# Kernel tuning notes

Hardware: AMD Instinct MI355X
Metric: run time of the kernel (lower is better)

The kernel has to match this reference:

```python
import jax, jax.numpy as jnp
import numpy as np

BETA_MIN = 1e-06


def setup_inputs() -> dict:
    key = jax.random.key(0)
    ks = jax.random.split(key, 4)
    B, H, W, C = 32, 56, 56, 256
    x = jax.random.normal(ks[0], (B, H, W, C), dtype=jnp.float32)
    # NonNeg-constrained weights, init value gamma_init = 1/16
    gamma_k = jax.random.uniform(ks[1], (1, 1, 8, C), dtype=jnp.float32) * (1.0 / 16.0)
    gamma_s = jax.random.uniform(ks[2], (3, 3, C, 1), dtype=jnp.float32) * (1.0 / 16.0)
    beta = jax.random.uniform(ks[3], (C,), dtype=jnp.float32) * 1e-06
    beta_outside = jnp.zeros((C,), dtype=jnp.float32)
    gamma_outside = jnp.ones((C,), dtype=jnp.float32)
    return {
        'x': x,
        'gamma_k': gamma_k,
        'gamma_s': gamma_s,
        'beta': beta,
        'beta_outside': beta_outside,
        'gamma_outside': gamma_outside,
        'surround_dist': 1,
    }


def reference(x, gamma_k, gamma_s, beta, beta_outside, gamma_outside, surround_dist):
    B, H, W, C = x.shape
    G = C // 8  # norm_groups = C / 8, 8 channels per group

    x2 = x * x

    # Grouped 1x1 conv: gamma_k[0,0] is [8, C]; group g uses columns g*8:(g+1)*8
    # reshape to [in=8, group, out=8] and contract per group.
    w = gamma_k[0, 0].reshape(8, G, 8)  # [i, g, o]
    Pk = jnp.einsum('bhwgi,igo->bhwgo', x2.reshape(B, H, W, G, 8), w)
    Pk = Pk.reshape(B, H, W, C)

    # Masked (center-zero) dilated 3x3 depthwise conv on squared inputs.
    mask = jnp.array([[1.0, 1.0, 1.0], [1.0, 0.0, 1.0], [1.0, 1.0, 1.0]], dtype=x.dtype)
    k = gamma_s[..., 0] * mask[:, :, None]  # [3, 3, C]
    kern = k[:, :, None, :]  # HWIO with I = C/groups = 1, O = C
    Ps = jax.lax.conv_general_dilated(
        x2, kern,
        window_strides=(1, 1),
        padding='SAME',
        rhs_dilation=(surround_dist, surround_dist),
        dimension_numbers=('NHWC', 'HWIO', 'NHWC'),
        feature_group_count=C,
    )

    # Divisive normalization: x / sqrt(Pk + Ps + beta + beta_min), then affine.
    norm_pool = jnp.reciprocal(jnp.sqrt(Pk + Ps + (beta + BETA_MIN)))
    return x * norm_pool * gamma_outside + beta_outside
```

## Files before the change

### kernel.cpp

```cpp
#include <hip/hip_runtime.h>

typedef float floatx4 __attribute__((ext_vector_type(4)));

#define BB 32
#define HH 56
#define WW 56
#define CC 256
#define PSTRIP 4
#define WSTRIPS 14
#define HTILE 4
#define HTILES 14
#define BLOCKS_PER_IMG (HTILES * WSTRIPS)

__global__ __launch_bounds__(256) void dn_kernel(
    const float* __restrict__ x,
    const float* __restrict__ gk_g,
    const float* __restrict__ gs_g,
    const float* __restrict__ beta,
    const float* __restrict__ beta_o,
    const float* __restrict__ gamma_o,
    const int* __restrict__ sdist,
    float* __restrict__ out)
{
    __shared__ float lw[20 * CC];

    const int tid = threadIdx.x;

    for (int idx = tid; idx < 19 * 64; idx += 256) {
        const int r  = idx >> 6;
        const int cq = (idx & 63) << 2;
        floatx4 v;
        if (r < 8) {
            v = *reinterpret_cast<const floatx4*>(gk_g + r * CC + cq);
        } else if (r < 16) {
            const int t   = r - 8;
            const int pos = t + (t >= 4 ? 1 : 0);
            v = *reinterpret_cast<const floatx4*>(gs_g + pos * CC + cq);
        } else if (r == 16) {
            v = *reinterpret_cast<const floatx4*>(beta + cq);
            v += 1e-6f;
        } else if (r == 17) {
            v = *reinterpret_cast<const floatx4*>(gamma_o + cq);
        } else {
            v = *reinterpret_cast<const floatx4*>(beta_o + cq);
        }
        *reinterpret_cast<floatx4*>(&lw[r * CC + cq]) = v;
    }

    const int d    = sdist[0];
    const int xcd  = blockIdx.x & 7;
    const int q    = blockIdx.x >> 3;
    const int b    = xcd + ((q / BLOCKS_PER_IMG) << 3);
    const int t0   = q % BLOCKS_PER_IMG;
    const int h    = (t0 / WSTRIPS) * HTILE + (tid >> 6);
    const int w0   = (t0 % WSTRIPS) * PSTRIP;
    const int lane = tid & 63;
    const int c0   = lane << 2;
    const int cg   = c0 & ~7;

    const float* xb   = x + (size_t)b * HH * WW * CC;
    const float* row0 = xb + (size_t)h * WW * CC;
    float*       orow = out + ((size_t)(b * HH + h) * WW) * CC;
    const float* wk   = lw + c0;

    const int  hm  = h - d, hp = h + d;
    const bool rmv = (unsigned)hm < HH;
    const bool rpv = (unsigned)hp < HH;
    const float* rowm = xb + (long)hm * (WW * CC);
    const float* rowp = xb + (long)hp * (WW * CC);
    const int cdm = -d * CC;
    const int cdp =  d * CC;

    __syncthreads();

    const floatx4 zero = {0.f, 0.f, 0.f, 0.f};

#pragma unroll
    for (int j = 0; j < PSTRIP; ++j) {
        const int w = w0 + j;
        const bool wmv = (w - d) >= 0;
        const bool wpv = (w + d) < WW;
        const float* cp = row0 + w * CC;
        const float* mp = rowm + w * CC;
        const float* pp = rowp + w * CC;

        floatx4 cxa = *reinterpret_cast<const floatx4*>(cp + cg);
        floatx4 cxb = *reinterpret_cast<const floatx4*>(cp + cg + 4);

        floatx4 tp[4];
        tp[0] = (rmv && wmv) ? *reinterpret_cast<const floatx4*>(mp + cdm + c0) : zero;
        tp[1] =  rmv         ? *reinterpret_cast<const floatx4*>(mp       + c0) : zero;
        tp[2] = (rmv && wpv) ? *reinterpret_cast<const floatx4*>(mp + cdp + c0) : zero;
        tp[3] =         wmv  ? *reinterpret_cast<const floatx4*>(cp + cdm + c0) : zero;

        const floatx4 cxo = (lane & 1) ? cxb : cxa;
        const floatx4 sqa = cxa * cxa, sqb = cxb * cxb;
        floatx4 acc = *reinterpret_cast<const floatx4*>(wk + 16 * CC);
#pragma unroll
        for (int i = 0; i < 4; ++i)
            acc += sqa[i] * *reinterpret_cast<const floatx4*>(wk + i * CC);
#pragma unroll
        for (int i = 0; i < 4; ++i)
            acc += sqb[i] * *reinterpret_cast<const floatx4*>(wk + (4 + i) * CC);

#pragma unroll
        for (int tt = 0; tt < 4; ++tt)
            acc += (tp[tt] * tp[tt]) *
                   *reinterpret_cast<const floatx4*>(wk + (8 + tt) * CC);

        tp[0] =         wpv  ? *reinterpret_cast<const floatx4*>(cp + cdp + c0) : zero;
        tp[1] = (rpv && wmv) ? *reinterpret_cast<const floatx4*>(pp + cdm + c0) : zero;
        tp[2] =  rpv         ? *reinterpret_cast<const floatx4*>(pp       + c0) : zero;
        tp[3] = (rpv && wpv) ? *reinterpret_cast<const floatx4*>(pp + cdp + c0) : zero;

#pragma unroll
        for (int tt = 0; tt < 4; ++tt)
            acc += (tp[tt] * tp[tt]) *
                   *reinterpret_cast<const floatx4*>(wk + (12 + tt) * CC);

        const floatx4 gov = *reinterpret_cast<const floatx4*>(wk + 17 * CC);
        const floatx4 bov = *reinterpret_cast<const floatx4*>(wk + 18 * CC);
        floatx4 res;
#pragma unroll
        for (int o = 0; o < 4; ++o)
            res[o] = cxo[o] * __builtin_amdgcn_rsqf(acc[o]) * gov[o] + bov[o];

        __builtin_nontemporal_store(res,
            reinterpret_cast<floatx4*>(orow + w * CC + c0));
    }
}

extern "C" void kernel_launch(void* const* d_in, const int* in_sizes, int n_in,
                              void* d_out, int out_size, void* d_ws, size_t ws_size,
                              hipStream_t stream) {
    const float* x       = (const float*)d_in[0];
    const float* gamma_k = (const float*)d_in[1];
    const float* gamma_s = (const float*)d_in[2];
    const float* beta    = (const float*)d_in[3];
    const float* beta_o  = (const float*)d_in[4];
    const float* gamma_o = (const float*)d_in[5];
    const int*   sdist   = (const int*)d_in[6];
    float* out = (float*)d_out;

    const int blocks = BB * BLOCKS_PER_IMG;
    dn_kernel<<<blocks, 256, 0, stream>>>(x, gamma_k, gamma_s, beta,
                                          beta_o, gamma_o, sdist, out);
}
```

Measured before the change: 227.6 us.

## Split channels across two waves per row and make neighbor loads branchless

Each wavefront now handles half of the channels at two channels per lane, and the tile height drops from four rows to two, which doubles the number of blocks. The eight neighbor loads for the depthwise stencil are now unconditional: their indices are clamped and the loaded values are multiplied by 0/1 validity masks instead of being loaded under a branch. The aim is more parallelism, lower register pressure and no divergent predicated loads. In exchange, loads narrow to 8 bytes, the weight table is loaded from global memory into LDS for twice as many blocks, and out-of-range loads are redundant but remain in bounds.

Result: slower. 263.2 us (+15.6%).

```diff
diff --git a/kernel.cpp b/kernel.cpp
--- a/kernel.cpp
+++ b/kernel.cpp
@@ -1,6 +1,7 @@
 #include <hip/hip_runtime.h>
 
 typedef float floatx4 __attribute__((ext_vector_type(4)));
+typedef float floatx2 __attribute__((ext_vector_type(2)));
 
 #define BB 32
 #define HH 56
@@ -8,8 +9,8 @@
 #define CC 256
 #define PSTRIP 4
 #define WSTRIPS 14
-#define HTILE 4
-#define HTILES 14
+#define HTILE 2
+#define HTILES 28
 #define BLOCKS_PER_IMG (HTILES * WSTRIPS)
 
 __global__ __launch_bounds__(256) void dn_kernel(
@@ -52,81 +53,89 @@
     const int q    = blockIdx.x >> 3;
     const int b    = xcd + ((q / BLOCKS_PER_IMG) << 3);
     const int t0   = q % BLOCKS_PER_IMG;
-    const int h    = (t0 / WSTRIPS) * HTILE + (tid >> 6);
+    const int wid  = tid >> 6;
+    const int h    = (t0 / WSTRIPS) * HTILE + (wid >> 1);
     const int w0   = (t0 % WSTRIPS) * PSTRIP;
+    const int half = wid & 1;
     const int lane = tid & 63;
-    const int c0   = lane << 2;
+    const int c0   = (half << 7) + (lane << 1);
     const int cg   = c0 & ~7;
 
-    const float* xb   = x + (size_t)b * HH * WW * CC;
-    const float* row0 = xb + (size_t)h * WW * CC;
+    const float* xb = x + (size_t)b * HH * WW * CC;
+
+    const int hm  = h - d, hp = h + d;
+    const float vrm = (hm >= 0) ? 1.f : 0.f;
+    const float vrp = (hp < HH) ? 1.f : 0.f;
+    const int hmc = (hm >= 0) ? hm : 0;
+    const int hpc = (hp < HH) ? hp : (HH - 1);
+    const float* rowm = xb + (size_t)hmc * (WW * CC);
+    const float* row0 = xb + (size_t)h   * (WW * CC);
+    const float* rowp = xb + (size_t)hpc * (WW * CC);
     float*       orow = out + ((size_t)(b * HH + h) * WW) * CC;
     const float* wk   = lw + c0;
 
-    const int  hm  = h - d, hp = h + d;
-    const bool rmv = (unsigned)hm < HH;
-    const bool rpv = (unsigned)hp < HH;
-    const float* rowm = xb + (long)hm * (WW * CC);
-    const float* rowp = xb + (long)hp * (WW * CC);
-    const int cdm = -d * CC;
-    const int cdp =  d * CC;
-
     __syncthreads();
-
-    const floatx4 zero = {0.f, 0.f, 0.f, 0.f};
 
 #pragma unroll
     for (int j = 0; j < PSTRIP; ++j) {
-        const int w = w0 + j;
-        const bool wmv = (w - d) >= 0;
-        const bool wpv = (w + d) < WW;
-        const float* cp = row0 + w * CC;
-        const float* mp = rowm + w * CC;
-        const float* pp = rowp + w * CC;
+        const int w  = w0 + j;
+        const int wm = w - d, wp = w + d;
+        const float vwm = (wm >= 0) ? 1.f : 0.f;
+        const float vwp = (wp < WW) ? 1.f : 0.f;
+        const int wmc = (wm >= 0) ? wm : 0;
+        const int wpc = (wp < WW) ? wp : (WW - 1);
+        const int colm = wmc * CC + c0;
+        const int col0 = w   * CC + c0;
+        const int colp = wpc * CC + c0;
 
-        floatx4 cxa = *reinterpret_cast<const floatx4*>(cp + cg);
-        floatx4 cxb = *reinterpret_cast<const floatx4*>(cp + cg + 4);
+        floatx2 t0v = *reinterpret_cast<const floatx2*>(rowm + colm);
+        floatx2 t1v = *reinterpret_cast<const floatx2*>(rowm + col0);
+        floatx2 t2v = *reinterpret_cast<const floatx2*>(rowm + colp);
+        floatx2 t3v = *reinterpret_cast<const floatx2*>(row0 + colm);
+        floatx2 t4v = *reinterpret_cast<const floatx2*>(row0 + colp);
+        floatx2 t5v = *reinterpret_cast<const floatx2*>(rowp + colm);
+        floatx2 t6v = *reinterpret_cast<const floatx2*>(rowp + col0);
+        floatx2 t7v = *reinterpret_cast<const floatx2*>(rowp + colp);
+        const float* cbase = row0 + w * CC + cg;
+        floatx4 cxa = *reinterpret_cast<const floatx4*>(cbase);
+        floatx4 cxb = *reinterpret_cast<const floatx4*>(cbase + 4);
 
-        floatx4 tp[4];
-        tp[0] = (rmv && wmv) ? *reinterpret_cast<const floatx4*>(mp + cdm + c0) : zero;
-        tp[1] =  rmv         ? *reinterpret_cast<const floatx4*>(mp       + c0) : zero;
-        tp[2] = (rmv && wpv) ? *reinterpret_cast<const floatx4*>(mp + cdp + c0) : zero;
-        tp[3] =         wmv  ? *reinterpret_cast<const floatx4*>(cp + cdm + c0) : zero;
+        const float m0 = vrm * vwm, m2 = vrm * vwp;
+        const float m5 = vrp * vwm, m7 = vrp * vwp;
 
-        const floatx4 cxo = (lane & 1) ? cxb : cxa;
+        const floatx4 s4 = (lane & 2) ? cxb : cxa;
+        floatx2 cxo;
+        cxo[0] = (lane & 1) ? s4[2] : s4[0];
+        cxo[1] = (lane & 1) ? s4[3] : s4[1];
         const floatx4 sqa = cxa * cxa, sqb = cxb * cxb;
-        floatx4 acc = *reinterpret_cast<const floatx4*>(wk + 16 * CC);
+
+        floatx2 acc = *reinterpret_cast<const floatx2*>(wk + 16 * CC);
 #pragma unroll
         for (int i = 0; i < 4; ++i)
-            acc += sqa[i] * *reinterpret_cast<const floatx4*>(wk + i * CC);
+            acc += sqa[i] * *reinterpret_cast<const floatx2*>(wk + i * CC);
 #pragma unroll
         for (int i = 0; i < 4; ++i)
-            acc += sqb[i] * *reinterpret_cast<const floatx4*>(wk + (4 + i) * CC);
+            acc += sqb[i] * *reinterpret_cast<const floatx2*>(wk + (4 + i) * CC);
 
-#pragma unroll
-        for (int tt = 0; tt < 4; ++tt)
-            acc += (tp[tt] * tp[tt]) *
-                   *reinterpret_cast<const floatx4*>(wk + (8 + tt) * CC);
+        t0v *= m0;  t1v *= vrm; t2v *= m2;  t3v *= vwm;
+        t4v *= vwp; t5v *= m5;  t6v *= vrp; t7v *= m7;
+        acc += (t0v * t0v) * *reinterpret_cast<const floatx2*>(wk +  8 * CC);
+        acc += (t1v * t1v) * *reinterpret_cast<const floatx2*>(wk +  9 * CC);
+        acc += (t2v * t2v) * *reinterpret_cast<const floatx2*>(wk + 10 * CC);
+        acc += (t3v * t3v) * *reinterpret_cast<const floatx2*>(wk + 11 * CC);
+        acc += (t4v * t4v) * *reinterpret_cast<const floatx2*>(wk + 12 * CC);
+        acc += (t5v * t5v) * *reinterpret_cast<const floatx2*>(wk + 13 * CC);
+        acc += (t6v * t6v) * *reinterpret_cast<const floatx2*>(wk + 14 * CC);
+        acc += (t7v * t7v) * *reinterpret_cast<const floatx2*>(wk + 15 * CC);
 
-        tp[0] =         wpv  ? *reinterpret_cast<const floatx4*>(cp + cdp + c0) : zero;
-        tp[1] = (rpv && wmv) ? *reinterpret_cast<const floatx4*>(pp + cdm + c0) : zero;
-        tp[2] =  rpv         ? *reinterpret_cast<const floatx4*>(pp       + c0) : zero;
-        tp[3] = (rpv && wpv) ? *reinterpret_cast<const floatx4*>(pp + cdp + c0) : zero;
+        const floatx2 gov = *reinterpret_cast<const floatx2*>(wk + 17 * CC);
+        const floatx2 bov = *reinterpret_cast<const floatx2*>(wk + 18 * CC);
+        floatx2 res;
+        res[0] = cxo[0] * __builtin_amdgcn_rsqf(acc[0]) * gov[0] + bov[0];
+        res[1] = cxo[1] * __builtin_amdgcn_rsqf(acc[1]) * gov[1] + bov[1];
 
-#pragma unroll
-        for (int tt = 0; tt < 4; ++tt)
-            acc += (tp[tt] * tp[tt]) *
-                   *reinterpret_cast<const floatx4*>(wk + (12 + tt) * CC);
-
-        const floatx4 gov = *reinterpret_cast<const floatx4*>(wk + 17 * CC);
-        const floatx4 bov = *reinterpret_cast<const floatx4*>(wk + 18 * CC);
-        floatx4 res;
-#pragma unroll
-        for (int o = 0; o < 4; ++o)
-            res[o] = cxo[o] * __builtin_amdgcn_rsqf(acc[o]) * gov[o] + bov[o];
-
-        __builtin_nontemporal_store(res,
-            reinterpret_cast<floatx4*>(orow + w * CC + c0));
+        floatx2* dst = reinterpret_cast<floatx2*>(orow + w * CC + c0);
+        __builtin_nontemporal_store(res, dst);
     }
 }
 
```
